# Kernel tuning notes

Hardware: AMD Instinct MI355X
Metric: run time of the kernel (lower is better)

## Reference

```python
import jax, jax.numpy as jnp
import numpy as np

B, C, IC, H, W = 4, 64, 32, 128, 128


def _conv1x1(x, w, b):
    # x: [b,c,h,w], w: [o,c], b: [o]
    return jnp.einsum('bchw,oc->bohw', x, w) + b[None, :, None, None]


def _maxpool2(x):
    b, c, h, w = x.shape
    return x.reshape(b, c, h // 2, 2, w // 2, 2).max(axis=(3, 5))


def setup_inputs() -> dict:
    key = jax.random.key(0)
    ks = jax.random.split(key, 11)
    sc = 0.05
    return {
        'target': jax.random.normal(ks[0], (B, C, H, W), jnp.float32),
        'ref': jax.random.normal(ks[1], (B, C, H, W), jnp.float32),
        'ref_align': jax.random.normal(ks[2], (B, C, H, W), jnp.float32),
        'theta_w': jax.random.normal(ks[3], (IC, C), jnp.float32) * sc,
        'theta_b': jax.random.normal(ks[4], (IC,), jnp.float32) * sc,
        'phi_w': jax.random.normal(ks[5], (IC, C), jnp.float32) * sc,
        'phi_b': jax.random.normal(ks[6], (IC,), jnp.float32) * sc,
        'g_w': jax.random.normal(ks[7], (IC, C), jnp.float32) * sc,
        'g_b': jax.random.normal(ks[8], (IC,), jnp.float32) * sc,
        'W_w': jax.random.normal(ks[9], (C, IC), jnp.float32) * sc,
        'W_b': jax.random.normal(ks[10], (C,), jnp.float32) * sc,
    }


def reference(target, ref, ref_align, theta_w, theta_b, phi_w, phi_b, g_w, g_b, W_w, W_b):
    b, c, h, w = target.shape
    N = h * w
    # phi, g: 1x1 conv then 2x2 maxpool -> [b, ic, N/4]
    phi = _maxpool2(_conv1x1(ref, phi_w, phi_b)).reshape(b, -1, N // 4)
    g = _maxpool2(_conv1x1(ref_align, g_w, g_b)).reshape(b, -1, N // 4)
    theta = _conv1x1(target, theta_w, theta_b).reshape(b, -1, N)  # [b, ic, N]
    # softmax-free attention: s [b, N, N/4]
    s = jnp.einsum('bin,bim->bnm', theta, phi) / N
    y = jnp.einsum('bnm,bim->bin', s, g)  # [b, ic, N]
    y = y.reshape(b, -1, h, w)
    return _conv1x1(y, W_w, W_b) + target
```

## Files before the change

kernel.cpp:

```cpp
#include <hip/hip_runtime.h>

#define Bn  4
#define Cc  64
#define ICc 32
#define Hh  128
#define Ww  128
#define Nn  (Hh*Ww)
#define Hp  (Hh/2)
#define Wp  (Ww/2)
#define Mm  (Hp*Wp)
#define Sg  8

__global__ __launch_bounds__(128) void conv_pool_kernel(
    const float* __restrict__ ref, const float* __restrict__ ref_align,
    const float* __restrict__ phi_w, const float* __restrict__ phi_b,
    const float* __restrict__ g_w,   const float* __restrict__ g_b,
    float* __restrict__ P, float* __restrict__ G)
{
    const int z   = blockIdx.z;
    const int inp = z & 1;
    const int icb = (z >> 1) * 8;
    const float* in   = inp ? ref_align : ref;
    const float* wmat = (inp ? g_w : phi_w) + icb * Cc;
    const float* bias = (inp ? g_b : phi_b) + icb;
    float* outp       = inp ? G : P;

    __shared__ float sw[8 * Cc];
    __shared__ float sb[8];
    for (int idx = threadIdx.x; idx < 8 * Cc; idx += 128) sw[idx] = wmat[idx];
    if (threadIdx.x < 8) sb[threadIdx.x] = bias[threadIdx.x];
    __syncthreads();

    const int tid = threadIdx.x;
    const int pw  = tid >> 1;
    const int r   = tid & 1;
    const int ph  = blockIdx.x;
    const int b   = blockIdx.y;
    const int hh  = 2 * ph + r;

    const float2* xrow = (const float2*)(in + ((size_t)b * Cc * Hh + hh) * Ww);
    const int cstride2 = (Hh * Ww) / 2;

    float acc0[8], acc1[8];
    #pragma unroll
    for (int i = 0; i < 8; ++i) { acc0[i] = sb[i]; acc1[i] = sb[i]; }

    #pragma unroll 8
    for (int c = 0; c < Cc; ++c) {
        float2 v = xrow[c * cstride2 + pw];
        #pragma unroll
        for (int i = 0; i < 8; ++i) {
            acc0[i] = fmaf(sw[i * Cc + c], v.x, acc0[i]);
            acc1[i] = fmaf(sw[i * Cc + c], v.y, acc1[i]);
        }
    }

    const int m = ph * Wp + pw;
    #pragma unroll
    for (int i = 0; i < 8; ++i) {
        float mx = fmaxf(acc0[i], acc1[i]);
        mx = fmaxf(mx, __shfl_xor(mx, 1, 64));
        if (r == 0) outp[((size_t)(b * ICc + icb + i)) * Mm + m] = mx;
    }
}

__global__ __launch_bounds__(256) void gram_kernel(
    const float* __restrict__ P, const float* __restrict__ G,
    float* __restrict__ Apart)
{
    const int i = blockIdx.x, b = blockIdx.y, s = blockIdx.z;
    const float* Gi = G + ((size_t)(b * ICc + i)) * Mm;
    const float* Pb = P + (size_t)b * ICc * Mm;
    const int mbase = s * (Mm / Sg);

    float acc[ICc];
    #pragma unroll
    for (int j = 0; j < ICc; ++j) acc[j] = 0.f;

    #pragma unroll
    for (int k = 0; k < (Mm / Sg) / 256; ++k) {
        int m = mbase + k * 256 + threadIdx.x;
        float gv = Gi[m];
        #pragma unroll
        for (int j = 0; j < ICc; ++j) acc[j] = fmaf(gv, Pb[j * Mm + m], acc[j]);
    }

    #pragma unroll
    for (int j = 0; j < ICc; ++j) {
        #pragma unroll
        for (int off = 32; off > 0; off >>= 1)
            acc[j] += __shfl_xor(acc[j], off, 64);
    }

    __shared__ float red[4][ICc];
    const int lane = threadIdx.x & 63, wid = threadIdx.x >> 6;
    if (lane == 0)
        for (int j = 0; j < ICc; ++j) red[wid][j] = acc[j];
    __syncthreads();

    if (threadIdx.x < ICc) {
        float sum = red[0][threadIdx.x] + red[1][threadIdx.x]
                  + red[2][threadIdx.x] + red[3][threadIdx.x];
        Apart[(((size_t)b * Sg + s) * ICc + i) * ICc + threadIdx.x] = sum;
    }
}

__global__ __launch_bounds__(256) void apply_kernel(
    const float* __restrict__ x, const float* __restrict__ Apart,
    const float* __restrict__ theta_w, const float* __restrict__ theta_b,
    const float* __restrict__ W_w,     const float* __restrict__ W_b,
    float* __restrict__ out)
{
    const int b     = blockIdx.y;
    const int obase = blockIdx.z * 4;

    __shared__ float sA[ICc * ICc];
    __shared__ float sT[4 * ICc];
    __shared__ float sM[4 * Cc];
    __shared__ float sv[4];

    const float* Ab = Apart + (size_t)b * Sg * ICc * ICc;
    for (int idx = threadIdx.x; idx < ICc * ICc; idx += 256) {
        float sum = 0.f;
        #pragma unroll
        for (int s = 0; s < Sg; ++s) sum += Ab[s * ICc * ICc + idx];
        sA[idx] = sum;
    }
    __syncthreads();

    if (threadIdx.x < 4 * ICc) {
        const int ol = threadIdx.x >> 5, j = threadIdx.x & 31;
        const float* wr = W_w + (obase + ol) * ICc;
        float t = 0.f;
        #pragma unroll
        for (int i = 0; i < ICc; ++i) t = fmaf(wr[i], sA[i * ICc + j], t);
        sT[ol * ICc + j] = t;
    }
    __syncthreads();

    const float invN = 1.f / (float)Nn;
    {
        const int ol = threadIdx.x >> 6, c = threadIdx.x & 63;
        float s = 0.f;
        #pragma unroll
        for (int j = 0; j < ICc; ++j) s = fmaf(sT[ol * ICc + j], theta_w[j * Cc + c], s);
        sM[ol * Cc + c] = s * invN + ((obase + ol) == c ? 1.f : 0.f);
        if (threadIdx.x < 4) {
            float v = 0.f;
            #pragma unroll
            for (int j = 0; j < ICc; ++j) v = fmaf(sT[threadIdx.x * ICc + j], theta_b[j], v);
            sv[threadIdx.x] = v * invN + W_b[obase + threadIdx.x];
        }
    }
    __syncthreads();

    const int n2 = blockIdx.x * 256 + threadIdx.x;
    const float2* xb = (const float2*)(x + (size_t)b * Cc * Nn);
    float2*       ob = (float2*)(out + (size_t)b * Cc * Nn);

    float accx[4], accy[4];
    #pragma unroll
    for (int i = 0; i < 4; ++i) { accx[i] = sv[i]; accy[i] = sv[i]; }

    #pragma unroll 8
    for (int c = 0; c < Cc; ++c) {
        float2 xv = xb[c * (Nn / 2) + n2];
        #pragma unroll
        for (int i = 0; i < 4; ++i) {
            float w = sM[i * Cc + c];
            accx[i] = fmaf(w, xv.x, accx[i]);
            accy[i] = fmaf(w, xv.y, accy[i]);
        }
    }

    #pragma unroll
    for (int i = 0; i < 4; ++i) {
        float2 o2; o2.x = accx[i]; o2.y = accy[i];
        ob[(obase + i) * (Nn / 2) + n2] = o2;
    }
}

extern "C" void kernel_launch(void* const* d_in, const int* in_sizes, int n_in,
                              void* d_out, int out_size, void* d_ws, size_t ws_size,
                              hipStream_t stream) {
    const float* target    = (const float*)d_in[0];
    const float* ref       = (const float*)d_in[1];
    const float* ref_align = (const float*)d_in[2];
    const float* theta_w   = (const float*)d_in[3];
    const float* theta_b   = (const float*)d_in[4];
    const float* phi_w     = (const float*)d_in[5];
    const float* phi_b     = (const float*)d_in[6];
    const float* g_w       = (const float*)d_in[7];
    const float* g_b       = (const float*)d_in[8];
    const float* W_w       = (const float*)d_in[9];
    const float* W_b       = (const float*)d_in[10];
    float* out = (float*)d_out;

    float* ws    = (float*)d_ws;
    float* P     = ws;
    float* G     = P + (size_t)Bn * ICc * Mm;
    float* Apart = G + (size_t)Bn * ICc * Mm;

    conv_pool_kernel<<<dim3(Hp, Bn, 8), 128, 0, stream>>>(ref, ref_align,
                                                          phi_w, phi_b, g_w, g_b, P, G);
    gram_kernel<<<dim3(ICc, Bn, Sg), 256, 0, stream>>>(P, G, Apart);
    apply_kernel<<<dim3(Nn / 512, Bn, 16), 256, 0, stream>>>(target, Apart,
                                                             theta_w, theta_b,
                                                             W_w, W_b, out);
}
```

Before: 151.0 us.

## Fuse three kernels into one cooperative kernel with grid-wide syncs

Merges the conv-pool, gram and apply kernels into a single cooperative launch of 512 blocks, separated by grid.sync, with a fallback to three launches if the cooperative launch fails. The per-block work is also reshaped: each block now does 16 output channels in conv and apply (larger register tiles), and gram processes two rows with float2 loads over a single 512-element slice per block. This targets launch overhead and inter-kernel gaps, at the cost of fewer, larger blocks (512 instead of 2048 in apply), higher register pressure and the cost of grid barriers.

```diff
diff --git a/kernel.cpp b/kernel.cpp
--- a/kernel.cpp
+++ b/kernel.cpp
@@ -1,4 +1,7 @@
 #include <hip/hip_runtime.h>
+#include <hip/hip_cooperative_groups.h>
+
+namespace cg = cooperative_groups;
 
 #define Bn  4
 #define Cc  64
@@ -11,173 +14,233 @@
 #define Mm  (Hp*Wp)
 #define Sg  8
 
-__global__ __launch_bounds__(128) void conv_pool_kernel(
+struct SharedMem {
+    float sw[ICc * Cc];
+    float sb[ICc];
+    float red[4][64];
+    float sA[ICc * ICc];
+    float sT[16 * ICc];
+    float sM[16 * Cc];
+    float sv[16];
+};
+
+__device__ void phase1(SharedMem& sm, int bid, int tid,
+                       const float* __restrict__ ref, const float* __restrict__ ref_align,
+                       const float* __restrict__ phi_w, const float* __restrict__ phi_b,
+                       const float* __restrict__ g_w,   const float* __restrict__ g_b,
+                       float* __restrict__ P, float* __restrict__ G)
+{
+    const int inp = bid & 1;
+    const int b   = (bid >> 1) & 3;
+    const int ph  = bid >> 3;
+    const float* in   = inp ? ref_align : ref;
+    const float* wmat = inp ? g_w : phi_w;
+    const float* bias = inp ? g_b : phi_b;
+    float* outp       = inp ? G : P;
+
+    for (int idx = tid; idx < ICc * Cc; idx += 256) sm.sw[idx] = wmat[idx];
+    if (tid < ICc) sm.sb[tid] = bias[tid];
+    __syncthreads();
+
+    const int icb = (tid >> 7) * 16;
+    const int t   = tid & 127;
+    const int pw  = t >> 1;
+    const int r   = t & 1;
+    const int hh  = 2 * ph + r;
+    const float2* xrow = (const float2*)(in + ((size_t)b * Cc * Hh + hh) * Ww);
+    const int cs2 = (Hh * Ww) / 2;
+
+    float acc0[16], acc1[16];
+    #pragma unroll
+    for (int i = 0; i < 16; ++i) { acc0[i] = sm.sb[icb + i]; acc1[i] = sm.sb[icb + i]; }
+
+    #pragma unroll 8
+    for (int c = 0; c < Cc; ++c) {
+        float2 v = xrow[c * cs2 + pw];
+        #pragma unroll
+        for (int i = 0; i < 16; ++i) {
+            float w = sm.sw[(icb + i) * Cc + c];
+            acc0[i] = fmaf(w, v.x, acc0[i]);
+            acc1[i] = fmaf(w, v.y, acc1[i]);
+        }
+    }
+
+    const int m = ph * Wp + pw;
+    #pragma unroll
+    for (int i = 0; i < 16; ++i) {
+        float mx = fmaxf(acc0[i], acc1[i]);
+        mx = fmaxf(mx, __shfl_xor(mx, 1, 64));
+        if (r == 0) outp[((size_t)(b * ICc + icb + i)) * Mm + m] = mx;
+    }
+}
+
+__device__ void phase2(SharedMem& sm, int bid, int tid,
+                       const float* __restrict__ P, const float* __restrict__ G,
+                       float* __restrict__ Apart)
+{
+    const int ig = bid & 15;
+    const int b  = (bid >> 4) & 3;
+    const int sl = bid >> 6;
+    const int i0 = ig * 2;
+    const int m2 = sl * 256 + tid;
+    const int cm2 = Mm / 2;
+    const float2* Gb = (const float2*)(G + (size_t)b * ICc * Mm);
+    const float2* Pb = (const float2*)(P + (size_t)b * ICc * Mm);
+
+    const float2 g0 = Gb[(i0 + 0) * cm2 + m2];
+    const float2 g1 = Gb[(i0 + 1) * cm2 + m2];
+
+    float a0[ICc], a1[ICc];
+    #pragma unroll 8
+    for (int j = 0; j < ICc; ++j) {
+        float2 p = Pb[j * cm2 + m2];
+        a0[j] = fmaf(g0.x, p.x, g0.y * p.y);
+        a1[j] = fmaf(g1.x, p.x, g1.y * p.y);
+    }
+
+    #pragma unroll
+    for (int j = 0; j < ICc; ++j) {
+        #pragma unroll
+        for (int off = 32; off > 0; off >>= 1) {
+            a0[j] += __shfl_xor(a0[j], off, 64);
+            a1[j] += __shfl_xor(a1[j], off, 64);
+        }
+    }
+
+    const int lane = tid & 63, wid = tid >> 6;
+    if (lane == 0) {
+        #pragma unroll
+        for (int j = 0; j < ICc; ++j) {
+            sm.red[wid][j]       = a0[j];
+            sm.red[wid][32 + j]  = a1[j];
+        }
+    }
+    __syncthreads();
+
+    if (tid < 64) {
+        float s = sm.red[0][tid] + sm.red[1][tid] + sm.red[2][tid] + sm.red[3][tid];
+        Apart[((size_t)(b * Sg + sl)) * (ICc * ICc) + (i0 + (tid >> 5)) * ICc + (tid & 31)] = s;
+    }
+    __syncthreads();
+}
+
+__device__ void phase3(SharedMem& sm, int bid, int tid,
+                       const float* __restrict__ x, const float* __restrict__ Apart,
+                       const float* __restrict__ theta_w, const float* __restrict__ theta_b,
+                       const float* __restrict__ W_w,     const float* __restrict__ W_b,
+                       float* __restrict__ out)
+{
+    const int nt = bid & 31;
+    const int b  = (bid >> 5) & 3;
+    const int ob = (bid >> 7) * 16;
+
+    const float* Ab = Apart + (size_t)b * Sg * ICc * ICc;
+    for (int idx = tid; idx < ICc * ICc; idx += 256) {
+        float s = 0.f;
+        #pragma unroll
+        for (int k = 0; k < Sg; ++k) s += Ab[k * ICc * ICc + idx];
+        sm.sA[idx] = s;
+    }
+    __syncthreads();
+
+    for (int idx = tid; idx < 16 * ICc; idx += 256) {
+        const int ol = idx >> 5, j = idx & 31;
+        const float* wr = W_w + (ob + ol) * ICc;
+        float t = 0.f;
+        #pragma unroll
+        for (int i = 0; i < ICc; ++i) t = fmaf(wr[i], sm.sA[i * ICc + j], t);
+        sm.sT[idx] = t;
+    }
+    __syncthreads();
+
+    const float invN = 1.f / (float)Nn;
+    for (int idx = tid; idx < 16 * Cc; idx += 256) {
+        const int ol = idx >> 6, c = idx & 63;
+        float s = 0.f;
+        #pragma unroll
+        for (int j = 0; j < ICc; ++j) s = fmaf(sm.sT[ol * ICc + j], theta_w[j * Cc + c], s);
+        sm.sM[idx] = s * invN + ((ob + ol) == c ? 1.f : 0.f);
+    }
+    if (tid < 16) {
+        float v = 0.f;
+        #pragma unroll
+        for (int j = 0; j < ICc; ++j) v = fmaf(sm.sT[tid * ICc + j], theta_b[j], v);
+        sm.sv[tid] = v * invN + W_b[ob + tid];
+    }
+    __syncthreads();
+
+    const int n2 = nt * 256 + tid;
+    const float2* xb = (const float2*)(x + (size_t)b * Cc * Nn);
+    float2*       ob2 = (float2*)(out + (size_t)b * Cc * Nn);
+
+    float ax[16], ay[16];
+    #pragma unroll
+    for (int i = 0; i < 16; ++i) { ax[i] = sm.sv[i]; ay[i] = sm.sv[i]; }
+
+    #pragma unroll 8
+    for (int c = 0; c < Cc; ++c) {
+        float2 xv = xb[c * (Nn / 2) + n2];
+        #pragma unroll
+        for (int i = 0; i < 16; ++i) {
+            float w = sm.sM[i * Cc + c];
+            ax[i] = fmaf(w, xv.x, ax[i]);
+            ay[i] = fmaf(w, xv.y, ay[i]);
+        }
+    }
+
+    #pragma unroll
+    for (int i = 0; i < 16; ++i) {
+        float2 o2; o2.x = ax[i]; o2.y = ay[i];
+        ob2[(ob + i) * (Nn / 2) + n2] = o2;
+    }
+}
+
+__global__ __launch_bounds__(256, 2) void mega_kernel(
+    const float* __restrict__ target, const float* __restrict__ ref,
+    const float* __restrict__ ref_align,
+    const float* __restrict__ theta_w, const float* __restrict__ theta_b,
+    const float* __restrict__ phi_w,   const float* __restrict__ phi_b,
+    const float* __restrict__ g_w,     const float* __restrict__ g_b,
+    const float* __restrict__ W_w,     const float* __restrict__ W_b,
+    float* __restrict__ P, float* __restrict__ G, float* __restrict__ Apart,
+    float* __restrict__ out)
+{
+    __shared__ SharedMem sm;
+    cg::grid_group grid = cg::this_grid();
+    const int bid = blockIdx.x, tid = threadIdx.x;
+
+    phase1(sm, bid, tid, ref, ref_align, phi_w, phi_b, g_w, g_b, P, G);
+    grid.sync();
+    phase2(sm, bid, tid, P, G, Apart);
+    grid.sync();
+    phase3(sm, bid, tid, target, Apart, theta_w, theta_b, W_w, W_b, out);
+}
+
+__global__ __launch_bounds__(256, 2) void k_conv(
     const float* __restrict__ ref, const float* __restrict__ ref_align,
     const float* __restrict__ phi_w, const float* __restrict__ phi_b,
     const float* __restrict__ g_w,   const float* __restrict__ g_b,
     float* __restrict__ P, float* __restrict__ G)
 {
-    const int z   = blockIdx.z;
-    const int inp = z & 1;
-    const int icb = (z >> 1) * 8;
-    const float* in   = inp ? ref_align : ref;
-    const float* wmat = (inp ? g_w : phi_w) + icb * Cc;
-    const float* bias = (inp ? g_b : phi_b) + icb;
-    float* outp       = inp ? G : P;
-
-    __shared__ float sw[8 * Cc];
-    __shared__ float sb[8];
-    for (int idx = threadIdx.x; idx < 8 * Cc; idx += 128) sw[idx] = wmat[idx];
-    if (threadIdx.x < 8) sb[threadIdx.x] = bias[threadIdx.x];
-    __syncthreads();
-
-    const int tid = threadIdx.x;
-    const int pw  = tid >> 1;
-    const int r   = tid & 1;
-    const int ph  = blockIdx.x;
-    const int b   = blockIdx.y;
-    const int hh  = 2 * ph + r;
-
-    const float2* xrow = (const float2*)(in + ((size_t)b * Cc * Hh + hh) * Ww);
-    const int cstride2 = (Hh * Ww) / 2;
-
-    float acc0[8], acc1[8];
-    #pragma unroll
-    for (int i = 0; i < 8; ++i) { acc0[i] = sb[i]; acc1[i] = sb[i]; }
-
-    #pragma unroll 8
-    for (int c = 0; c < Cc; ++c) {
-        float2 v = xrow[c * cstride2 + pw];
-        #pragma unroll
-        for (int i = 0; i < 8; ++i) {
-            acc0[i] = fmaf(sw[i * Cc + c], v.x, acc0[i]);
-            acc1[i] = fmaf(sw[i * Cc + c], v.y, acc1[i]);
-        }
-    }
-
-    const int m = ph * Wp + pw;
-    #pragma unroll
-    for (int i = 0; i < 8; ++i) {
-        float mx = fmaxf(acc0[i], acc1[i]);
-        mx = fmaxf(mx, __shfl_xor(mx, 1, 64));
-        if (r == 0) outp[((size_t)(b * ICc + icb + i)) * Mm + m] = mx;
-    }
-}
-
-__global__ __launch_bounds__(256) void gram_kernel(
-    const float* __restrict__ P, const float* __restrict__ G,
-    float* __restrict__ Apart)
-{
-    const int i = blockIdx.x, b = blockIdx.y, s = blockIdx.z;
-    const float* Gi = G + ((size_t)(b * ICc + i)) * Mm;
-    const float* Pb = P + (size_t)b * ICc * Mm;
-    const int mbase = s * (Mm / Sg);
-
-    float acc[ICc];
-    #pragma unroll
-    for (int j = 0; j < ICc; ++j) acc[j] = 0.f;
-
-    #pragma unroll
-    for (int k = 0; k < (Mm / Sg) / 256; ++k) {
-        int m = mbase + k * 256 + threadIdx.x;
-        float gv = Gi[m];
-        #pragma unroll
-        for (int j = 0; j < ICc; ++j) acc[j] = fmaf(gv, Pb[j * Mm + m], acc[j]);
-    }
-
-    #pragma unroll
-    for (int j = 0; j < ICc; ++j) {
-        #pragma unroll
-        for (int off = 32; off > 0; off >>= 1)
-            acc[j] += __shfl_xor(acc[j], off, 64);
-    }
-
-    __shared__ float red[4][ICc];
-    const int lane = threadIdx.x & 63, wid = threadIdx.x >> 6;
-    if (lane == 0)
-        for (int j = 0; j < ICc; ++j) red[wid][j] = acc[j];
-    __syncthreads();
-
-    if (threadIdx.x < ICc) {
-        float sum = red[0][threadIdx.x] + red[1][threadIdx.x]
-                  + red[2][threadIdx.x] + red[3][threadIdx.x];
-        Apart[(((size_t)b * Sg + s) * ICc + i) * ICc + threadIdx.x] = sum;
-    }
-}
-
-__global__ __launch_bounds__(256) void apply_kernel(
+    __shared__ SharedMem sm;
+    phase1(sm, blockIdx.x, threadIdx.x, ref, ref_align, phi_w, phi_b, g_w, g_b, P, G);
+}
+
+__global__ __launch_bounds__(256, 2) void k_gram(
+    const float* __restrict__ P, const float* __restrict__ G, float* __restrict__ Apart)
+{
+    __shared__ SharedMem sm;
+    phase2(sm, blockIdx.x, threadIdx.x, P, G, Apart);
+}
+
+__global__ __launch_bounds__(256, 2) void k_apply(
     const float* __restrict__ x, const float* __restrict__ Apart,
     const float* __restrict__ theta_w, const float* __restrict__ theta_b,
     const float* __restrict__ W_w,     const float* __restrict__ W_b,
     float* __restrict__ out)
 {
-    const int b     = blockIdx.y;
-    const int obase = blockIdx.z * 4;
-
-    __shared__ float sA[ICc * ICc];
-    __shared__ float sT[4 * ICc];
-    __shared__ float sM[4 * Cc];
-    __shared__ float sv[4];
-
-    const float* Ab = Apart + (size_t)b * Sg * ICc * ICc;
-    for (int idx = threadIdx.x; idx < ICc * ICc; idx += 256) {
-        float sum = 0.f;
-        #pragma unroll
-        for (int s = 0; s < Sg; ++s) sum += Ab[s * ICc * ICc + idx];
-        sA[idx] = sum;
-    }
-    __syncthreads();
-
-    if (threadIdx.x < 4 * ICc) {
-        const int ol = threadIdx.x >> 5, j = threadIdx.x & 31;
-        const float* wr = W_w + (obase + ol) * ICc;
-        float t = 0.f;
-        #pragma unroll
-        for (int i = 0; i < ICc; ++i) t = fmaf(wr[i], sA[i * ICc + j], t);
-        sT[ol * ICc + j] = t;
-    }
-    __syncthreads();
-
-    const float invN = 1.f / (float)Nn;
-    {
-        const int ol = threadIdx.x >> 6, c = threadIdx.x & 63;
-        float s = 0.f;
-        #pragma unroll
-        for (int j = 0; j < ICc; ++j) s = fmaf(sT[ol * ICc + j], theta_w[j * Cc + c], s);
-        sM[ol * Cc + c] = s * invN + ((obase + ol) == c ? 1.f : 0.f);
-        if (threadIdx.x < 4) {
-            float v = 0.f;
-            #pragma unroll
-            for (int j = 0; j < ICc; ++j) v = fmaf(sT[threadIdx.x * ICc + j], theta_b[j], v);
-            sv[threadIdx.x] = v * invN + W_b[obase + threadIdx.x];
-        }
-    }
-    __syncthreads();
-
-    const int n2 = blockIdx.x * 256 + threadIdx.x;
-    const float2* xb = (const float2*)(x + (size_t)b * Cc * Nn);
-    float2*       ob = (float2*)(out + (size_t)b * Cc * Nn);
-
-    float accx[4], accy[4];
-    #pragma unroll
-    for (int i = 0; i < 4; ++i) { accx[i] = sv[i]; accy[i] = sv[i]; }
-
-    #pragma unroll 8
-    for (int c = 0; c < Cc; ++c) {
-        float2 xv = xb[c * (Nn / 2) + n2];
-        #pragma unroll
-        for (int i = 0; i < 4; ++i) {
-            float w = sM[i * Cc + c];
-            accx[i] = fmaf(w, xv.x, accx[i]);
-            accy[i] = fmaf(w, xv.y, accy[i]);
-        }
-    }
-
-    #pragma unroll
-    for (int i = 0; i < 4; ++i) {
-        float2 o2; o2.x = accx[i]; o2.y = accy[i];
-        ob[(obase + i) * (Nn / 2) + n2] = o2;
-    }
+    __shared__ SharedMem sm;
+    phase3(sm, blockIdx.x, threadIdx.x, x, Apart, theta_w, theta_b, W_w, W_b, out);
 }
 
 extern "C" void kernel_launch(void* const* d_in, const int* in_sizes, int n_in,
@@ -201,10 +264,18 @@
     float* G     = P + (size_t)Bn * ICc * Mm;
     float* Apart = G + (size_t)Bn * ICc * Mm;
 
-    conv_pool_kernel<<<dim3(Hp, Bn, 8), 128, 0, stream>>>(ref, ref_align,
-                                                          phi_w, phi_b, g_w, g_b, P, G);
-    gram_kernel<<<dim3(ICc, Bn, Sg), 256, 0, stream>>>(P, G, Apart);
-    apply_kernel<<<dim3(Nn / 512, Bn, 16), 256, 0, stream>>>(target, Apart,
-                                                             theta_w, theta_b,
-                                                             W_w, W_b, out);
-}
+    void* args[] = {
+        (void*)&target, (void*)&ref, (void*)&ref_align,
+        (void*)&theta_w, (void*)&theta_b, (void*)&phi_w, (void*)&phi_b,
+        (void*)&g_w, (void*)&g_b, (void*)&W_w, (void*)&W_b,
+        (void*)&P, (void*)&G, (void*)&Apart, (void*)&out
+    };
+    hipError_t e = hipLaunchCooperativeKernel(
+        reinterpret_cast<void*>(mega_kernel), dim3(512), dim3(256), args, 0, stream);
+
+    if (e != hipSuccess) {
+        k_conv<<<512, 256, 0, stream>>>(ref, ref_align, phi_w, phi_b, g_w, g_b, P, G);
+        k_gram<<<512, 256, 0, stream>>>(P, G, Apart);
+        k_apply<<<512, 256, 0, stream>>>(target, Apart, theta_w, theta_b, W_w, W_b, out);
+    }
+}
```

After: 307.3 us. 103% more time.

## Raise per-block channel reuse in conv and apply, vectorize gram with float4

Applied to the files above, without the earlier changes.

The conv-pool kernel now uses 256-thread blocks that each cover 16 output channels, and the apply kernel computes 8 output channels per block instead of 4. Both changes halve how many times the large input tensors are re-read from memory. The gram kernel loads float4 vectors and handles one float4 per thread over a 4-way split, which cuts the partial-sum count and the reduction work in apply. The cost is more registers per thread in apply and fewer blocks, so there is less parallelism to hide memory latency.

```diff
diff --git a/kernel.cpp b/kernel.cpp
--- a/kernel.cpp
+++ b/kernel.cpp
@@ -9,9 +9,9 @@
 #define Hp  (Hh/2)
 #define Wp  (Ww/2)
 #define Mm  (Hp*Wp)
-#define Sg  8
-
-__global__ __launch_bounds__(128) void conv_pool_kernel(
+#define Sg  4
+
+__global__ __launch_bounds__(256) void conv_pool_kernel(
     const float* __restrict__ ref, const float* __restrict__ ref_align,
     const float* __restrict__ phi_w, const float* __restrict__ phi_b,
     const float* __restrict__ g_w,   const float* __restrict__ g_b,
@@ -19,39 +19,41 @@
 {
     const int z   = blockIdx.z;
     const int inp = z & 1;
-    const int icb = (z >> 1) * 8;
+    const int ich = (z >> 1) * 16;
     const float* in   = inp ? ref_align : ref;
-    const float* wmat = (inp ? g_w : phi_w) + icb * Cc;
-    const float* bias = (inp ? g_b : phi_b) + icb;
+    const float* wmat = (inp ? g_w : phi_w) + ich * Cc;
+    const float* bias = (inp ? g_b : phi_b) + ich;
     float* outp       = inp ? G : P;
 
-    __shared__ float sw[8 * Cc];
-    __shared__ float sb[8];
-    for (int idx = threadIdx.x; idx < 8 * Cc; idx += 128) sw[idx] = wmat[idx];
-    if (threadIdx.x < 8) sb[threadIdx.x] = bias[threadIdx.x];
-    __syncthreads();
-
-    const int tid = threadIdx.x;
-    const int pw  = tid >> 1;
-    const int r   = tid & 1;
+    __shared__ float sw[16 * Cc];
+    __shared__ float sb[16];
+    for (int idx = threadIdx.x; idx < 16 * Cc; idx += 256) sw[idx] = wmat[idx];
+    if (threadIdx.x < 16) sb[threadIdx.x] = bias[threadIdx.x];
+    __syncthreads();
+
+    const int icq = (threadIdx.x >> 7) * 8;
+    const int t   = threadIdx.x & 127;
+    const int pw  = t >> 1;
+    const int r   = t & 1;
     const int ph  = blockIdx.x;
     const int b   = blockIdx.y;
     const int hh  = 2 * ph + r;
 
     const float2* xrow = (const float2*)(in + ((size_t)b * Cc * Hh + hh) * Ww);
-    const int cstride2 = (Hh * Ww) / 2;
+    const int cs2 = (Hh * Ww) / 2;
 
     float acc0[8], acc1[8];
     #pragma unroll
-    for (int i = 0; i < 8; ++i) { acc0[i] = sb[i]; acc1[i] = sb[i]; }
+    for (int i = 0; i < 8; ++i) { acc0[i] = sb[icq + i]; acc1[i] = sb[icq + i]; }
 
     #pragma unroll 8
     for (int c = 0; c < Cc; ++c) {
-        float2 v = xrow[c * cstride2 + pw];
+        float2 v = xrow[c * cs2 + pw];
         #pragma unroll
         for (int i = 0; i < 8; ++i) {
-            acc0[i] = fmaf(sw[i * Cc + c], v.x, acc0[i]);
-            acc1[i] = fmaf(sw[i * Cc + c], v.y, acc1[i]);
+            float w = sw[(icq + i) * Cc + c];
+            acc0[i] = fmaf(w, v.x, acc0[i]);
+            acc1[i] = fmaf(w, v.y, acc1[i]);
         }
     }
 
@@ -60,7 +62,7 @@
     for (int i = 0; i < 8; ++i) {
         float mx = fmaxf(acc0[i], acc1[i]);
         mx = fmaxf(mx, __shfl_xor(mx, 1, 64));
-        if (r == 0) outp[((size_t)(b * ICc + icb + i)) * Mm + m] = mx;
+        if (r == 0) outp[((size_t)(b * ICc + ich + icq + i)) * Mm + m] = mx;
     }
 }
 
@@ -69,20 +71,18 @@
     float* __restrict__ Apart)
 {
     const int i = blockIdx.x, b = blockIdx.y, s = blockIdx.z;
-    const float* Gi = G + ((size_t)(b * ICc + i)) * Mm;
-    const float* Pb = P + (size_t)b * ICc * Mm;
-    const int mbase = s * (Mm / Sg);
+    const int cm4 = Mm / 4;
+    const int q   = s * 256 + threadIdx.x;
+    const float4* G4 = (const float4*)(G + (size_t)b * ICc * Mm);
+    const float4* P4 = (const float4*)(P + (size_t)b * ICc * Mm);
+
+    const float4 g = G4[i * cm4 + q];
 
     float acc[ICc];
-    #pragma unroll
-    for (int j = 0; j < ICc; ++j) acc[j] = 0.f;
-
-    #pragma unroll
-    for (int k = 0; k < (Mm / Sg) / 256; ++k) {
-        int m = mbase + k * 256 + threadIdx.x;
-        float gv = Gi[m];
-        #pragma unroll
-        for (int j = 0; j < ICc; ++j) acc[j] = fmaf(gv, Pb[j * Mm + m], acc[j]);
+    #pragma unroll 8
+    for (int j = 0; j < ICc; ++j) {
+        float4 p = P4[j * cm4 + q];
+        acc[j] = fmaf(g.x, p.x, fmaf(g.y, p.y, fmaf(g.z, p.z, g.w * p.w)));
     }
 
     #pragma unroll
@@ -111,26 +111,26 @@
     const float* __restrict__ W_w,     const float* __restrict__ W_b,
     float* __restrict__ out)
 {
-    const int b     = blockIdx.y;
-    const int obase = blockIdx.z * 4;
+    const int b  = blockIdx.y;
+    const int ob = blockIdx.z * 8;
 
     __shared__ float sA[ICc * ICc];
-    __shared__ float sT[4 * ICc];
-    __shared__ float sM[4 * Cc];
-    __shared__ float sv[4];
+    __shared__ float sT[8 * ICc];
+    __shared__ float sM[8 * Cc];
+    __shared__ float sv[8];
 
     const float* Ab = Apart + (size_t)b * Sg * ICc * ICc;
     for (int idx = threadIdx.x; idx < ICc * ICc; idx += 256) {
-        float sum = 0.f;
-        #pragma unroll
-        for (int s = 0; s < Sg; ++s) sum += Ab[s * ICc * ICc + idx];
-        sA[idx] = sum;
-    }
-    __syncthreads();
-
-    if (threadIdx.x < 4 * ICc) {
+        float s = 0.f;
+        #pragma unroll
+        for (int k = 0; k < Sg; ++k) s += Ab[k * ICc * ICc + idx];
+        sA[idx] = s;
+    }
+    __syncthreads();
+
+    {
         const int ol = threadIdx.x >> 5, j = threadIdx.x & 31;
-        const float* wr = W_w + (obase + ol) * ICc;
+        const float* wr = W_w + (ob + ol) * ICc;
         float t = 0.f;
         #pragma unroll
         for (int i = 0; i < ICc; ++i) t = fmaf(wr[i], sA[i * ICc + j], t);
@@ -139,44 +139,44 @@
     __syncthreads();
 
     const float invN = 1.f / (float)Nn;
-    {
-        const int ol = threadIdx.x >> 6, c = threadIdx.x & 63;
+    for (int idx = threadIdx.x; idx < 8 * Cc; idx += 256) {
+        const int ol = idx >> 6, c = idx & 63;
         float s = 0.f;
         #pragma unroll
         for (int j = 0; j < ICc; ++j) s = fmaf(sT[ol * ICc + j], theta_w[j * Cc + c], s);
-        sM[ol * Cc + c] = s * invN + ((obase + ol) == c ? 1.f : 0.f);
-        if (threadIdx.x < 4) {
-            float v = 0.f;
-            #pragma unroll
-            for (int j = 0; j < ICc; ++j) v = fmaf(sT[threadIdx.x * ICc + j], theta_b[j], v);
-            sv[threadIdx.x] = v * invN + W_b[obase + threadIdx.x];
-        }
+        sM[idx] = s * invN + ((ob + ol) == c ? 1.f : 0.f);
+    }
+    if (threadIdx.x < 8) {
+        float v = 0.f;
+        #pragma unroll
+        for (int j = 0; j < ICc; ++j) v = fmaf(sT[threadIdx.x * ICc + j], theta_b[j], v);
+        sv[threadIdx.x] = v * invN + W_b[ob + threadIdx.x];
     }
     __syncthreads();
 
     const int n2 = blockIdx.x * 256 + threadIdx.x;
-    const float2* xb = (const float2*)(x + (size_t)b * Cc * Nn);
-    float2*       ob = (float2*)(out + (size_t)b * Cc * Nn);
-
-    float accx[4], accy[4];
-    #pragma unroll
-    for (int i = 0; i < 4; ++i) { accx[i] = sv[i]; accy[i] = sv[i]; }
+    const float2* xb  = (const float2*)(x + (size_t)b * Cc * Nn);
+    float2*       ob2 = (float2*)(out + (size_t)b * Cc * Nn);
+
+    float ax[8], ay[8];
+    #pragma unroll
+    for (int i = 0; i < 8; ++i) { ax[i] = sv[i]; ay[i] = sv[i]; }
 
     #pragma unroll 8
     for (int c = 0; c < Cc; ++c) {
         float2 xv = xb[c * (Nn / 2) + n2];
         #pragma unroll
-        for (int i = 0; i < 4; ++i) {
+        for (int i = 0; i < 8; ++i) {
             float w = sM[i * Cc + c];
-            accx[i] = fmaf(w, xv.x, accx[i]);
-            accy[i] = fmaf(w, xv.y, accy[i]);
+            ax[i] = fmaf(w, xv.x, ax[i]);
+            ay[i] = fmaf(w, xv.y, ay[i]);
         }
     }
 
     #pragma unroll
-    for (int i = 0; i < 4; ++i) {
-        float2 o2; o2.x = accx[i]; o2.y = accy[i];
-        ob[(obase + i) * (Nn / 2) + n2] = o2;
+    for (int i = 0; i < 8; ++i) {
+        float2 o2; o2.x = ax[i]; o2.y = ay[i];
+        ob2[(ob + i) * (Nn / 2) + n2] = o2;
     }
 }
 
@@ -201,10 +201,10 @@
     float* G     = P + (size_t)Bn * ICc * Mm;
     float* Apart = G + (size_t)Bn * ICc * Mm;
 
-    conv_pool_kernel<<<dim3(Hp, Bn, 8), 128, 0, stream>>>(ref, ref_align,
+    conv_pool_kernel<<<dim3(Hp, Bn, 4), 256, 0, stream>>>(ref, ref_align,
                                                           phi_w, phi_b, g_w, g_b, P, G);
     gram_kernel<<<dim3(ICc, Bn, Sg), 256, 0, stream>>>(P, G, Apart);
-    apply_kernel<<<dim3(Nn / 512, Bn, 16), 256, 0, stream>>>(target, Apart,
-                                                             theta_w, theta_b,
-                                                             W_w, W_b, out);
-}
+    apply_kernel<<<dim3(Nn / 512, Bn, 8), 256, 0, stream>>>(target, Apart,
+                                                            theta_w, theta_b,
+                                                            W_w, W_b, out);
+}
```

Result: faster. 147.6 us (-2.2%).
